# Kernel optimization log

Measured on AMD Instinct MI355X. Metric: run time of the kernel, lower is better.

Reference implementation:

```python
import math
import jax, jax.numpy as jnp
import numpy as np

B, N, D, H = 4, 2048, 512, 8
HD = D // H


def setup_inputs() -> dict:
    key = jax.random.key(0)
    ks = jax.random.split(key, 7)
    w_scale = 1.0 / math.sqrt(D)  # keep logits in a sane range (like default init)
    return {
        "q": jax.random.normal(ks[0], (B, N, D), dtype=jnp.float32),
        "mask": jax.random.randint(ks[1], (B, N), 0, 2) == 1,  # True = masked key
        "attn_bias": jax.random.normal(ks[2], (B, N, N), dtype=jnp.float32),
        "Wq": jax.random.normal(ks[3], (D, D), dtype=jnp.float32) * w_scale,
        "Wk": jax.random.normal(ks[4], (D, D), dtype=jnp.float32) * w_scale,
        "Wv": jax.random.normal(ks[5], (D, D), dtype=jnp.float32) * w_scale,
        "Wo": jax.random.normal(ks[6], (D, D), dtype=jnp.float32) * w_scale,
    }


def _heads(v):
    # [B, N, D] -> [H, B, N, HD]  (mirrors reshape + movedim(-2, 0))
    b, n, d = v.shape
    return v.reshape(b, n, H, HD).transpose(2, 0, 1, 3)


def reference(q, mask, attn_bias, Wq, Wk, Wv, Wo):
    # Linear projections (torch Linear: x @ W.T)
    qh = _heads(q @ Wq.T)
    kh = _heads(q @ Wk.T)   # self-attention: h defaults to q
    vh = _heads(q @ Wv.T)
    # scores: [H, B, Nq, Nk]
    scores = jnp.einsum("hbqd,hbkd->hbqk", qh, kh) / math.sqrt(HD)
    scores = scores + attn_bias[None]                     # broadcast over heads
    scores = jnp.where(mask[None, :, None, :], -jnp.inf, scores)
    attn = jax.nn.softmax(scores, axis=-1)
    out = jnp.einsum("hbqk,hbkd->hbqd", attn, vh)         # [H, B, Nq, HD]
    out = out.transpose(1, 2, 0, 3).reshape(q.shape[0], q.shape[1], D)
    return out @ Wo.T
```

## Files before the change

### kernel.cpp

```cpp
#include <hip/hip_runtime.h>
#include <stdint.h>


typedef __attribute__((ext_vector_type(8))) short short8;
typedef __attribute__((ext_vector_type(4))) short short4v;
typedef __attribute__((ext_vector_type(4))) float f32x4;

#define DEV static __device__ __forceinline__

constexpr int Bc = 4, Nc = 2048, Dc = 512, Hc = 8, HDc = 64;
constexpr int Mc = Bc * Nc;
constexpr int QKVNc = 3 * Dc;
constexpr float L2E = 1.44269504f;

DEV short bf16cast(float f) {
  return (short)__builtin_bit_cast(unsigned short, (__bf16)f);
}
DEV unsigned cvt_pk_bf16(float a, float b) {
  unsigned short lb = __builtin_bit_cast(unsigned short, (__bf16)a);
  unsigned short hb = __builtin_bit_cast(unsigned short, (__bf16)b);
  return (unsigned)lb | ((unsigned)hb << 16);
}
DEV unsigned pack_shorts(short a, short b) {
  return (unsigned)(unsigned short)a | ((unsigned)(unsigned short)b << 16);
}
DEV float fast_exp2(float x) {
#if __has_builtin(__builtin_amdgcn_exp2f)
  return __builtin_amdgcn_exp2f(x);
#else
  return exp2f(x);
#endif
}
DEV void permswap32(unsigned& a, unsigned& b) {
  asm volatile("v_permlane32_swap_b32 %0, %1" : "+v"(a), "+v"(b));
}
DEV void gl_lds16(const short* g, short* l) {
  __builtin_amdgcn_global_load_lds(
      (const __attribute__((address_space(1))) void*)g,
      (__attribute__((address_space(3))) void*)l, 16, 0, 0);
}

__global__ void cvtw_kernel(const float* __restrict__ Wq, const float* __restrict__ Wk,
                            const float* __restrict__ Wv, const float* __restrict__ Wo,
                            const float* __restrict__ q,
                            short* __restrict__ Wqkv, short* __restrict__ Wob,
                            short* __restrict__ qb,
                            const void* __restrict__ mask, float* __restrict__ mf) {
  int bid = blockIdx.x;
  if (bid >= 5120) {
    __shared__ int flag;
    if (threadIdx.x == 0) flag = 0;
    __syncthreads();
    const uchar4* m4 = (const uchar4*)mask;
    int acc = 0;
    for (int i = threadIdx.x; i < 2048; i += 256) {
      uchar4 v = m4[i];
      acc |= (int)v.y | (int)v.z | (int)v.w;
    }
    if (acc) atomicOr(&flag, 1);
    __syncthreads();
    int isbyte = flag;
    for (int i = threadIdx.x; i < Bc * Nc; i += 256) {
      int v = isbyte ? (int)((const unsigned char*)mask)[i] : ((const int*)mask)[i];
      mf[i] = v ? -1e30f : 0.0f;
    }
    return;
  }
  const float* src; short* dst; int j;
  if (bid < 1024) {
    int which = bid >> 8;
    j = (bid & 255) * 256 + threadIdx.x;
    src = which == 0 ? Wq : which == 1 ? Wk : which == 2 ? Wv : Wo;
    dst = (which == 3) ? Wob : Wqkv + which * (Dc * Dc);
  } else {
    j = (bid - 1024) * 256 + threadIdx.x;
    src = q; dst = qb;
  }
  float4 v = ((const float4*)src)[j];
  short4v o = { bf16cast(v.x), bf16cast(v.y), bf16cast(v.z), bf16cast(v.w) };
  ((short4v*)dst)[j] = o;
}

template<int BN, bool OUT_F32, int MINW>
__global__ __launch_bounds__(256, MINW) void gemm_bt(const short* __restrict__ A,
                                                     const short* __restrict__ Bm,
                                                     void* __restrict__ Cv,
                                                     int M, int N, int K,
                                                     int qcols, float cscale) {
  constexpr int MT = (BN == 128) ? 4 : 2;
  constexpr int NT = 4;
  __shared__ __align__(16) short At[128 * 64];
  __shared__ __align__(16) short Bt[BN * 64];
  const int tid = threadIdx.x, lane = tid & 63, wv = tid >> 6;
  const int quad = lane >> 4, l16 = lane & 15;
  const int mbase = blockIdx.y * 128, nbase = blockIdx.x * BN;
  const int wr = (BN == 128) ? (wv >> 1) * 64 : wv * 32;
  const int wc = (BN == 128) ? (wv & 1) * 64 : 0;
  const float scale = (nbase < qcols) ? cscale : 1.0f;
  f32x4 acc[MT][NT] = {};

  for (int k0 = 0; k0 < K; k0 += 64) {
#pragma unroll
    for (int i = 0; i < 4; i++) {
      int ibase = (wv * 4 + i) * 64;
      int row = (ibase + lane) >> 3, c = lane & 7;
      gl_lds16(&A[(size_t)(mbase + row) * K + k0 + ((c ^ (row & 7)) << 3)],
               &At[ibase << 3]);
    }
#pragma unroll
    for (int i = 0; i < BN / 32; i++) {
      int ibase = (wv * (BN / 32) + i) * 64;
      int row = (ibase + lane) >> 3, c = lane & 7;
      gl_lds16(&Bm[(size_t)(nbase + row) * K + k0 + ((c ^ (row & 7)) << 3)],
               &Bt[ibase << 3]);
    }
    __syncthreads();
#pragma unroll
    for (int s = 0; s < 2; s++) {
      short8 af[MT], bf[NT];
#pragma unroll
      for (int t = 0; t < MT; t++) {
        int r = wr + t * 16 + l16;
        af[t] = *(short8*)&At[r * 64 + (((quad + 4 * s) ^ (r & 7)) << 3)];
      }
#pragma unroll
      for (int t = 0; t < NT; t++) {
        int r = wc + t * 16 + l16;
        bf[t] = *(short8*)&Bt[r * 64 + (((quad + 4 * s) ^ (r & 7)) << 3)];
      }
#pragma unroll
      for (int mt = 0; mt < MT; mt++)
#pragma unroll
        for (int nt = 0; nt < NT; nt++)
          acc[mt][nt] = __builtin_amdgcn_mfma_f32_16x16x32_bf16(af[mt], bf[nt], acc[mt][nt], 0, 0, 0);
    }
    __syncthreads();
  }
#pragma unroll
  for (int mt = 0; mt < MT; mt++)
#pragma unroll
    for (int nt = 0; nt < NT; nt++)
#pragma unroll
      for (int r = 0; r < 4; r++) {
        int row = mbase + wr + mt * 16 + quad * 4 + r;
        int col = nbase + wc + nt * 16 + l16;
        float v = acc[mt][nt][r] * scale;
        if (OUT_F32) ((float*)Cv)[(size_t)row * N + col] = v;
        else         ((short*)Cv)[(size_t)row * N + col] = bf16cast(v);
      }
}

__global__ __launch_bounds__(256, 2) void attn_kernel(const short* __restrict__ QKV,
                                                      const float* __restrict__ bias,
                                                      const float* __restrict__ maskf,
                                                      short* __restrict__ Aout) {
  __shared__ __align__(16) short Kt[2][64 * 64];
  __shared__ __align__(16) short Vt[2][64 * 64];
  __shared__ __align__(16) float mlds[Nc];
  const int tid = threadIdx.x, lane = tid & 63, wv = tid >> 6;
  const int quad = lane >> 4, l16 = lane & 15;
  const int qt = blockIdx.x & 15, h = (blockIdx.x >> 4) & 7, b = (int)(blockIdx.x >> 7);
  const int qrow0 = qt * 128;
  const int q0 = qrow0 + wv * 32 + l16;
  const float* biasq0 = bias + ((size_t)b * Nc + q0) * Nc;
  const float* biasq1 = biasq0 + (size_t)16 * Nc;

  ((float4*)mlds)[tid]       = ((const float4*)(maskf + b * Nc))[tid];
  ((float4*)mlds)[tid + 256] = ((const float4*)(maskf + b * Nc))[tid + 256];

  short8 qf[2][2];
  {
    const short* qp0 = QKV + (size_t)(b * Nc + q0) * QKVNc + h * HDc + quad * 8;
    qf[0][0] = *(const short8*)qp0;
    qf[0][1] = *(const short8*)(qp0 + 32);
    const short* qp1 = qp0 + (size_t)16 * QKVNc;
    qf[1][0] = *(const short8*)qp1;
    qf[1][1] = *(const short8*)(qp1 + 32);
  }

  const int krow = tid >> 2, kch0 = (tid & 3) * 2;
  const int kw0 = krow * 64 + ((kch0 ^ (krow & 7)) << 3);
  const int kw1 = krow * 64 + (((kch0 + 1) ^ (krow & 7)) << 3);
  const int vp = tid & 31, vq = tid >> 5;
  const int vperm = (vp & 25) | ((vp & 4) >> 1) | ((vp & 2) << 1);
  const int vwbase = (((vperm >> 2)) << 3) + 2 * (vperm & 3);
  const short* Kbase = QKV + Dc + h * HDc;
  const short* Vbase = QKV + 2 * Dc + h * HDc;

  short8 kpre0, kpre1, v0pre, v1pre;
  {
    const short* kp = &Kbase[(size_t)(b * Nc + krow) * QKVNc + kch0 * 8];
    kpre0 = *(const short8*)kp;
    kpre1 = *(const short8*)(kp + 8);
    v0pre = *(const short8*)&Vbase[(size_t)(b * Nc + 2 * vp) * QKVNc + vq * 8];
    v1pre = *(const short8*)&Vbase[(size_t)(b * Nc + 2 * vp + 1) * QKVNc + vq * 8];
  }

  const short ONEB = (short)0x3F80;
  const short8 ones = { ONEB, ONEB, ONEB, ONEB, ONEB, ONEB, ONEB, ONEB };

  f32x4 oacc[2][4] = {};
  f32x4 sumacc[2] = {};

  for (int kt = 0; kt < 32; kt++) {
    const int cur = kt & 1;
    const int kb = kt * 64;
    const int kbn = ((kt + 1) & 31) * 64;

    *(short8*)&Kt[cur][kw0] = kpre0;
    *(short8*)&Kt[cur][kw1] = kpre1;
#pragma unroll
    for (int j = 0; j < 8; j++) {
      int hd = vq * 8 + j;
      *(unsigned*)&Vt[cur][hd * 64 + (vwbase ^ ((hd & 7) << 3))] =
          pack_shorts(v0pre[j], v1pre[j]);
    }
    __syncthreads();

    {
      const short* kp = &Kbase[(size_t)(b * Nc + kbn + krow) * QKVNc + kch0 * 8];
      kpre0 = *(const short8*)kp;
      kpre1 = *(const short8*)(kp + 8);
      v0pre = *(const short8*)&Vbase[(size_t)(b * Nc + kbn + 2 * vp) * QKVNc + vq * 8];
      v1pre = *(const short8*)&Vbase[(size_t)(b * Nc + kbn + 2 * vp + 1) * QKVNc + vq * 8];
    }
    float4 bb[2][4];
#pragma unroll
    for (int t = 0; t < 4; t++) {
      bb[0][t] = *(const float4*)&biasq0[kb + t * 16 + quad * 4];
      bb[1][t] = *(const float4*)&biasq1[kb + t * 16 + quad * 4];
    }

    f32x4 sacc[2][4];
#pragma unroll
    for (int t = 0; t < 4; t++) {
      float4 mv = *(const float4*)&mlds[kb + t * 16 + quad * 4];
      sacc[0][t][0] = mv.x; sacc[0][t][1] = mv.y; sacc[0][t][2] = mv.z; sacc[0][t][3] = mv.w;
      sacc[1][t] = sacc[0][t];
    }

#pragma unroll
    for (int s = 0; s < 2; s++)
#pragma unroll
      for (int t = 0; t < 4; t++) {
        short8 kf = *(short8*)&Kt[cur][(t * 16 + l16) * 64 + (((quad + 4 * s) ^ (l16 & 7)) << 3)];
        sacc[0][t] = __builtin_amdgcn_mfma_f32_16x16x32_bf16(kf, qf[0][s], sacc[0][t], 0, 0, 0);
        sacc[1][t] = __builtin_amdgcn_mfma_f32_16x16x32_bf16(kf, qf[1][s], sacc[1][t], 0, 0, 0);
      }

    short8 pf[2][2];
#pragma unroll
    for (int n = 0; n < 2; n++) {
      unsigned pw[4][2];
#pragma unroll
      for (int t = 0; t < 4; t++) {
        float p0 = fast_exp2(__builtin_fmaf(bb[n][t].x, L2E, sacc[n][t][0]));
        float p1 = fast_exp2(__builtin_fmaf(bb[n][t].y, L2E, sacc[n][t][1]));
        float p2 = fast_exp2(__builtin_fmaf(bb[n][t].z, L2E, sacc[n][t][2]));
        float p3 = fast_exp2(__builtin_fmaf(bb[n][t].w, L2E, sacc[n][t][3]));
        pw[t][0] = cvt_pk_bf16(p0, p1);
        pw[t][1] = cvt_pk_bf16(p2, p3);
      }
      permswap32(pw[0][0], pw[1][0]); permswap32(pw[0][1], pw[1][1]);
      permswap32(pw[2][0], pw[3][0]); permswap32(pw[2][1], pw[3][1]);
      union { unsigned u[4]; short8 s; }
          a0{{pw[0][0], pw[0][1], pw[1][0], pw[1][1]}},
          a1{{pw[2][0], pw[2][1], pw[3][0], pw[3][1]}};
      pf[n][0] = a0.s; pf[n][1] = a1.s;
    }

#pragma unroll
    for (int s = 0; s < 2; s++) {
      sumacc[0] = __builtin_amdgcn_mfma_f32_16x16x32_bf16(pf[0][s], ones, sumacc[0], 0, 0, 0);
      sumacc[1] = __builtin_amdgcn_mfma_f32_16x16x32_bf16(pf[1][s], ones, sumacc[1], 0, 0, 0);
#pragma unroll
      for (int t = 0; t < 4; t++) {
        short8 vf = *(short8*)&Vt[cur][(t * 16 + l16) * 64 + (((quad + 4 * s) ^ (l16 & 7)) << 3)];
        oacc[0][t] = __builtin_amdgcn_mfma_f32_16x16x32_bf16(pf[0][s], vf, oacc[0][t], 0, 0, 0);
        oacc[1][t] = __builtin_amdgcn_mfma_f32_16x16x32_bf16(pf[1][s], vf, oacc[1][t], 0, 0, 0);
      }
    }
  }

#pragma unroll
  for (int m = 0; m < 2; m++)
#pragma unroll
    for (int r = 0; r < 4; r++) {
      float inv = 1.0f / sumacc[m][r];
      int row = b * Nc + qrow0 + wv * 32 + m * 16 + quad * 4 + r;
#pragma unroll
      for (int t = 0; t < 4; t++)
        Aout[(size_t)row * Dc + h * HDc + t * 16 + l16] = bf16cast(oacc[m][t][r] * inv);
    }
}

extern "C" void kernel_launch(void* const* d_in, const int* in_sizes, int n_in,
                              void* d_out, int out_size, void* d_ws, size_t ws_size,
                              hipStream_t stream) {
  const float* q    = (const float*)d_in[0];
  const void*  mask = d_in[1];
  const float* bias = (const float*)d_in[2];
  const float* Wq   = (const float*)d_in[3];
  const float* Wk   = (const float*)d_in[4];
  const float* Wv   = (const float*)d_in[5];
  const float* Wo   = (const float*)d_in[6];
  float* out = (float*)d_out;

  char* ws = (char*)d_ws;
  short* Wqkv = (short*)ws;  ws += (size_t)QKVNc * Dc * 2;
  short* Wob  = (short*)ws;  ws += (size_t)Dc * Dc * 2;
  float* mf   = (float*)ws;  ws += (size_t)Bc * Nc * 4;
  short* QKV  = (short*)ws;  ws += (size_t)Mc * QKVNc * 2;
  short* aout = (short*)ws;  ws += (size_t)Mc * Dc * 2;
  short* qb   = (short*)ws;  ws += (size_t)Mc * Dc * 2;

  cvtw_kernel<<<dim3(5121), dim3(256), 0, stream>>>(Wq, Wk, Wv, Wo, q, Wqkv, Wob, qb, mask, mf);

  gemm_bt<128, false, 3><<<dim3(QKVNc / 128, Mc / 128), dim3(256), 0, stream>>>(
      qb, Wqkv, (void*)QKV, Mc, QKVNc, Dc, Dc, 0.125f * L2E);
  attn_kernel<<<dim3(Bc * Hc * 16), dim3(256), 0, stream>>>(QKV, bias, mf, aout);
  gemm_bt<64, true, 4><<<dim3(Dc / 64, Mc / 128), dim3(256), 0, stream>>>(
      aout, Wob, (void*)out, Mc, Dc, Dc, 0, 1.0f);
}
```

Before: 269.5 us.

## Split attention key range in two with partial outputs and combine kernel

Each attention block now handles half of the keys, which doubles the grid to 1024 blocks and raises the launch-bounds occupancy target to 4 blocks per CU. Unnormalized fp32 partial outputs and row sums go to workspace, and a new combine kernel adds the two halves and normalizes them to bf16. Bias loads for the next tile are also prefetched one iteration ahead. The aim is better occupancy and latency hiding, paid for with extra fp32 partial traffic, an extra launch, and reuse of the qb workspace region for the partials.

Result: slower. 351.7 us (+30.5%).

```diff
diff --git a/kernel.cpp b/kernel.cpp
--- a/kernel.cpp
+++ b/kernel.cpp
@@ -12,6 +12,8 @@
 constexpr int Mc = Bc * Nc;
 constexpr int QKVNc = 3 * Dc;
 constexpr float L2E = 1.44269504f;
+constexpr size_t OP_HALF = (size_t)32 * 16 * 128 * 64;
+constexpr size_t RS_HALF = (size_t)32 * 16 * 128;
 
 DEV short bf16cast(float f) {
   return (short)__builtin_bit_cast(unsigned short, (__bf16)f);
@@ -150,23 +152,26 @@
       }
 }
 
-__global__ __launch_bounds__(256, 2) void attn_kernel(const short* __restrict__ QKV,
+__global__ __launch_bounds__(256, 4) void attn_kernel(const short* __restrict__ QKV,
                                                       const float* __restrict__ bias,
                                                       const float* __restrict__ maskf,
-                                                      short* __restrict__ Aout) {
+                                                      float* __restrict__ Opart,
+                                                      float* __restrict__ rsv) {
   __shared__ __align__(16) short Kt[2][64 * 64];
   __shared__ __align__(16) short Vt[2][64 * 64];
-  __shared__ __align__(16) float mlds[Nc];
+  __shared__ __align__(16) float mlds[1024];
   const int tid = threadIdx.x, lane = tid & 63, wv = tid >> 6;
   const int quad = lane >> 4, l16 = lane & 15;
-  const int qt = blockIdx.x & 15, h = (blockIdx.x >> 4) & 7, b = (int)(blockIdx.x >> 7);
+  const int half = blockIdx.x & 1;
+  const int rest = blockIdx.x >> 1;
+  const int qt = rest & 15, h = (rest >> 4) & 7, b = rest >> 7;
+  const int key0 = half * 1024;
   const int qrow0 = qt * 128;
   const int q0 = qrow0 + wv * 32 + l16;
-  const float* biasq0 = bias + ((size_t)b * Nc + q0) * Nc;
+  const float* biasq0 = bias + ((size_t)b * Nc + q0) * Nc + key0;
   const float* biasq1 = biasq0 + (size_t)16 * Nc;
 
-  ((float4*)mlds)[tid]       = ((const float4*)(maskf + b * Nc))[tid];
-  ((float4*)mlds)[tid + 256] = ((const float4*)(maskf + b * Nc))[tid + 256];
+  ((float4*)mlds)[tid] = ((const float4*)(maskf + b * Nc + key0))[tid];
 
   short8 qf[2][2];
   {
@@ -189,11 +194,17 @@
 
   short8 kpre0, kpre1, v0pre, v1pre;
   {
-    const short* kp = &Kbase[(size_t)(b * Nc + krow) * QKVNc + kch0 * 8];
+    const short* kp = &Kbase[(size_t)(b * Nc + key0 + krow) * QKVNc + kch0 * 8];
     kpre0 = *(const short8*)kp;
     kpre1 = *(const short8*)(kp + 8);
-    v0pre = *(const short8*)&Vbase[(size_t)(b * Nc + 2 * vp) * QKVNc + vq * 8];
-    v1pre = *(const short8*)&Vbase[(size_t)(b * Nc + 2 * vp + 1) * QKVNc + vq * 8];
+    v0pre = *(const short8*)&Vbase[(size_t)(b * Nc + key0 + 2 * vp) * QKVNc + vq * 8];
+    v1pre = *(const short8*)&Vbase[(size_t)(b * Nc + key0 + 2 * vp + 1) * QKVNc + vq * 8];
+  }
+  float4 bpre[2][4];
+#pragma unroll
+  for (int t = 0; t < 4; t++) {
+    bpre[0][t] = *(const float4*)&biasq0[t * 16 + quad * 4];
+    bpre[1][t] = *(const float4*)&biasq1[t * 16 + quad * 4];
   }
 
   const short ONEB = (short)0x3F80;
@@ -202,10 +213,10 @@
   f32x4 oacc[2][4] = {};
   f32x4 sumacc[2] = {};
 
-  for (int kt = 0; kt < 32; kt++) {
+  for (int kt = 0; kt < 16; kt++) {
     const int cur = kt & 1;
     const int kb = kt * 64;
-    const int kbn = ((kt + 1) & 31) * 64;
+    const int kbn = ((kt + 1) & 15) * 64;
 
     *(short8*)&Kt[cur][kw0] = kpre0;
     *(short8*)&Kt[cur][kw1] = kpre1;
@@ -218,17 +229,11 @@
     __syncthreads();
 
     {
-      const short* kp = &Kbase[(size_t)(b * Nc + kbn + krow) * QKVNc + kch0 * 8];
+      const short* kp = &Kbase[(size_t)(b * Nc + key0 + kbn + krow) * QKVNc + kch0 * 8];
       kpre0 = *(const short8*)kp;
       kpre1 = *(const short8*)(kp + 8);
-      v0pre = *(const short8*)&Vbase[(size_t)(b * Nc + kbn + 2 * vp) * QKVNc + vq * 8];
-      v1pre = *(const short8*)&Vbase[(size_t)(b * Nc + kbn + 2 * vp + 1) * QKVNc + vq * 8];
-    }
-    float4 bb[2][4];
-#pragma unroll
-    for (int t = 0; t < 4; t++) {
-      bb[0][t] = *(const float4*)&biasq0[kb + t * 16 + quad * 4];
-      bb[1][t] = *(const float4*)&biasq1[kb + t * 16 + quad * 4];
+      v0pre = *(const short8*)&Vbase[(size_t)(b * Nc + key0 + kbn + 2 * vp) * QKVNc + vq * 8];
+      v1pre = *(const short8*)&Vbase[(size_t)(b * Nc + key0 + kbn + 2 * vp + 1) * QKVNc + vq * 8];
     }
 
     f32x4 sacc[2][4];
@@ -254,10 +259,10 @@
       unsigned pw[4][2];
 #pragma unroll
       for (int t = 0; t < 4; t++) {
-        float p0 = fast_exp2(__builtin_fmaf(bb[n][t].x, L2E, sacc[n][t][0]));
-        float p1 = fast_exp2(__builtin_fmaf(bb[n][t].y, L2E, sacc[n][t][1]));
-        float p2 = fast_exp2(__builtin_fmaf(bb[n][t].z, L2E, sacc[n][t][2]));
-        float p3 = fast_exp2(__builtin_fmaf(bb[n][t].w, L2E, sacc[n][t][3]));
+        float p0 = fast_exp2(__builtin_fmaf(bpre[n][t].x, L2E, sacc[n][t][0]));
+        float p1 = fast_exp2(__builtin_fmaf(bpre[n][t].y, L2E, sacc[n][t][1]));
+        float p2 = fast_exp2(__builtin_fmaf(bpre[n][t].z, L2E, sacc[n][t][2]));
+        float p3 = fast_exp2(__builtin_fmaf(bpre[n][t].w, L2E, sacc[n][t][3]));
         pw[t][0] = cvt_pk_bf16(p0, p1);
         pw[t][1] = cvt_pk_bf16(p2, p3);
       }
@@ -270,6 +275,12 @@
     }
 
 #pragma unroll
+    for (int t = 0; t < 4; t++) {
+      bpre[0][t] = *(const float4*)&biasq0[kbn + t * 16 + quad * 4];
+      bpre[1][t] = *(const float4*)&biasq1[kbn + t * 16 + quad * 4];
+    }
+
+#pragma unroll
     for (int s = 0; s < 2; s++) {
       sumacc[0] = __builtin_amdgcn_mfma_f32_16x16x32_bf16(pf[0][s], ones, sumacc[0], 0, 0, 0);
       sumacc[1] = __builtin_amdgcn_mfma_f32_16x16x32_bf16(pf[1][s], ones, sumacc[1], 0, 0, 0);
@@ -282,16 +293,40 @@
     }
   }
 
+  const size_t blk = (size_t)(b * 8 + h) * 16 + qt;
+  float* Op = Opart + (size_t)half * OP_HALF + blk * (128 * 64);
+  float* Rs = rsv + (size_t)half * RS_HALF + blk * 128;
 #pragma unroll
   for (int m = 0; m < 2; m++)
 #pragma unroll
     for (int r = 0; r < 4; r++) {
-      float inv = 1.0f / sumacc[m][r];
-      int row = b * Nc + qrow0 + wv * 32 + m * 16 + quad * 4 + r;
+      int q = wv * 32 + m * 16 + quad * 4 + r;
 #pragma unroll
       for (int t = 0; t < 4; t++)
-        Aout[(size_t)row * Dc + h * HDc + t * 16 + l16] = bf16cast(oacc[m][t][r] * inv);
-    }
+        Op[(size_t)q * 64 + t * 16 + l16] = oacc[m][t][r];
+      if (l16 == 0) Rs[q] = sumacc[m][r];
+    }
+}
+
+__global__ __launch_bounds__(256) void combine_kernel(const float* __restrict__ Opart,
+                                                      const float* __restrict__ rsv,
+                                                      short* __restrict__ Aout) {
+  int idx = blockIdx.x * 256 + threadIdx.x;
+  int oct = idx & 7, hh = (idx >> 3) & 7, row = idx >> 6;
+  int b = row >> 11, qg = row & 2047;
+  int qt = qg >> 7, qq = qg & 127;
+  size_t blk = (size_t)(b * 8 + hh) * 16 + qt;
+  size_t base = (blk * 128 + qq) * 64 + (size_t)oct * 8;
+  float4 a0 = *(const float4*)&Opart[base];
+  float4 a1 = *(const float4*)&Opart[base + 4];
+  float4 c0 = *(const float4*)&Opart[OP_HALF + base];
+  float4 c1 = *(const float4*)&Opart[OP_HALF + base + 4];
+  float inv = 1.0f / (rsv[blk * 128 + qq] + rsv[RS_HALF + blk * 128 + qq]);
+  short8 o = { bf16cast((a0.x + c0.x) * inv), bf16cast((a0.y + c0.y) * inv),
+               bf16cast((a0.z + c0.z) * inv), bf16cast((a0.w + c0.w) * inv),
+               bf16cast((a1.x + c1.x) * inv), bf16cast((a1.y + c1.y) * inv),
+               bf16cast((a1.z + c1.z) * inv), bf16cast((a1.w + c1.w) * inv) };
+  *(short8*)&Aout[(size_t)row * Dc + hh * HDc + oct * 8] = o;
 }
 
 extern "C" void kernel_launch(void* const* d_in, const int* in_sizes, int n_in,
@@ -312,13 +347,17 @@
   float* mf   = (float*)ws;  ws += (size_t)Bc * Nc * 4;
   short* QKV  = (short*)ws;  ws += (size_t)Mc * QKVNc * 2;
   short* aout = (short*)ws;  ws += (size_t)Mc * Dc * 2;
-  short* qb   = (short*)ws;  ws += (size_t)Mc * Dc * 2;
+  char* ubase = ws;
+  short* qb    = (short*)ubase;
+  float* Opart = (float*)ubase;
+  float* rsv   = (float*)(ubase + OP_HALF * 2 * sizeof(float));
 
   cvtw_kernel<<<dim3(5121), dim3(256), 0, stream>>>(Wq, Wk, Wv, Wo, q, Wqkv, Wob, qb, mask, mf);
 
   gemm_bt<128, false, 3><<<dim3(QKVNc / 128, Mc / 128), dim3(256), 0, stream>>>(
       qb, Wqkv, (void*)QKV, Mc, QKVNc, Dc, Dc, 0.125f * L2E);
-  attn_kernel<<<dim3(Bc * Hc * 16), dim3(256), 0, stream>>>(QKV, bias, mf, aout);
+  attn_kernel<<<dim3(Bc * Hc * 16 * 2), dim3(256), 0, stream>>>(QKV, bias, mf, Opart, rsv);
+  combine_kernel<<<dim3(2048), dim3(256), 0, stream>>>(Opart, rsv, aout);
   gemm_bt<64, true, 4><<<dim3(Dc / 64, Mc / 128), dim3(256), 0, stream>>>(
       aout, Wob, (void*)out, Mc, Dc, Dc, 0, 1.0f);
 }
```
